# Kernel optimization log

Hardware: AMD Instinct MI355X
Metric: run time of the kernel (lower is better)

The kernel has to match this reference:

```python
import jax, jax.numpy as jnp
import numpy as np

E, N, D = 640000, 10000, 128  # edges, nodes, feature dim (edge=node=global=128)
H, O = 256, 128               # MLP hidden / output dims; concat dim = 4*D = 512


def setup_inputs() -> dict:
    key = jax.random.key(0)
    ks = jax.random.split(key, 7)
    return {
        "edge_attr": jax.random.normal(ks[0], (E, D), dtype=jnp.float32),
        "node_attr": jax.random.normal(ks[1], (N, D), dtype=jnp.float32),
        "global_attr": jax.random.normal(ks[2], (D,), dtype=jnp.float32),
        "senders": jax.random.randint(ks[3], (E,), 0, N),
        "receivers": jax.random.randint(ks[4], (E,), 0, N),
        "W1": jax.random.normal(ks[5], (4 * D, H), dtype=jnp.float32) / np.float32(np.sqrt(4 * D)),
        "b1": jnp.zeros((H,), dtype=jnp.float32),
        "W2": jax.random.normal(ks[6], (H, O), dtype=jnp.float32) / np.float32(np.sqrt(H)),
        "b2": jnp.zeros((O,), dtype=jnp.float32),
    }


def reference(edge_attr, node_attr, global_attr, senders, receivers, W1, b1, W2, b2):
    # Batched form of the per-edge Python loop:
    #   cat([e.data, e.receiver.data, e.sender.data, G.global_attribute.data]) -> updater MLP
    num_edges = edge_attr.shape[0]
    g = jnp.broadcast_to(global_attr, (num_edges, global_attr.shape[0]))  # [E, Dg]
    x = jnp.concatenate(
        [edge_attr, node_attr[receivers], node_attr[senders], g], axis=-1
    )  # [E, 4D]
    h = jax.nn.relu(x @ W1 + b1)  # [E, H]
    return h @ W2 + b2            # [E, O] : updated edge attributes
```

## Files before the change

kernel.cpp:

```cpp
#include <hip/hip_runtime.h>
#include <hip/hip_bf16.h>


typedef __attribute__((ext_vector_type(8))) short bf16x8;
typedef __attribute__((ext_vector_type(4))) float f32x4;

static __device__ __forceinline__ unsigned short f2bf(float f) {
    unsigned u = __builtin_bit_cast(unsigned, f);
    u += 0x7FFFu + ((u >> 16) & 1u);
    return (unsigned short)(u >> 16);
}


__global__ void prep_node_kernel(const float* __restrict__ node,
                                 ushort* __restrict__ nb) {
    int i = blockIdx.x * 256 + threadIdx.x;
    if (i >= 160000) return;
    const float4* s = (const float4*)(node + (size_t)i * 8);
    float4 a = s[0], b = s[1];
    ushort tmp[8] = { f2bf(a.x), f2bf(a.y), f2bf(a.z), f2bf(a.w),
                      f2bf(b.x), f2bf(b.y), f2bf(b.z), f2bf(b.w) };
    *(bf16x8*)&nb[(size_t)i * 8] = *(bf16x8*)tmp;
}

__global__ void prep_w1_kernel(const float* __restrict__ W1,
                               ushort* __restrict__ w1f) {
    int id = blockIdx.x * 256 + threadIdx.x;
    if (id >= 16 * 12 * 64) return;
    int l = id & 63, blk = id >> 6;
    int ks = blk % 12, gnt = blk / 12;
    int n  = gnt * 16 + (l & 15);
    int k0 = ks * 32 + (l >> 4) * 8;
    ushort tmp[8];
    #pragma unroll
    for (int j = 0; j < 8; ++j) tmp[j] = f2bf(W1[(k0 + j) * 256 + n]);
    *(bf16x8*)&w1f[(size_t)id * 8] = *(bf16x8*)tmp;
}

__global__ void prep_w2_kernel(const float* __restrict__ W2,
                               ushort* __restrict__ w2f) {
    int id = blockIdx.x * 256 + threadIdx.x;
    if (id >= 8 * 8 * 64) return;
    int l = id & 63, blk = id >> 6;
    int ks = blk % 8, gnt = blk / 8;
    int n  = gnt * 16 + (l & 15);
    int k0 = ks * 32 + (l >> 4) * 8;
    ushort tmp[8];
    #pragma unroll
    for (int j = 0; j < 8; ++j) tmp[j] = f2bf(W2[(k0 + j) * 128 + n]);
    *(bf16x8*)&w2f[(size_t)id * 8] = *(bf16x8*)tmp;
}

__global__ void prep_hbias_kernel(const float* __restrict__ W1,
                                  const float* __restrict__ b1,
                                  const float* __restrict__ g,
                                  float* __restrict__ hbias) {
    int n = threadIdx.x;
    float acc = b1[n];
    for (int k = 0; k < 128; ++k) acc += g[k] * W1[(384 + k) * 256 + n];
    hbias[n] = acc;
}


__global__ __launch_bounds__(256, 2) void edge_mlp_kernel(
    const float* __restrict__ edge_attr,
    const int* __restrict__ senders,
    const int* __restrict__ receivers,
    const ushort* __restrict__ node_bf,
    const ushort* __restrict__ w1f,
    const ushort* __restrict__ w2f,
    const float* __restrict__ hbias,
    const float* __restrict__ b2,
    float* __restrict__ out)
{
    __shared__ ushort Xe[64 * 128];
    __shared__ ushort Hs[64 * 256];

    const int t   = threadIdx.x;
    const int l   = t & 63;
    const int wid = t >> 6;
    const int base = blockIdx.x * 64;

    const int lr = l & 15;
    const int lk = (l >> 4) * 8;

    #pragma unroll
    for (int p = 0; p < 4; ++p) {
        int chunk = p * 256 + t;
        int r  = chunk >> 4;
        int c0 = (chunk & 15) * 8;
        const float4* src = (const float4*)(edge_attr + (size_t)(base + r) * 128 + c0);
        float4 a = src[0];
        float4 b = src[1];
        ushort tmp[8] = { f2bf(a.x), f2bf(a.y), f2bf(a.z), f2bf(a.w),
                          f2bf(b.x), f2bf(b.y), f2bf(b.z), f2bf(b.w) };
        *(bf16x8*)&Xe[r * 128 + (c0 ^ ((r & 7) << 3))] = *(bf16x8*)tmp;
    }

    int nrow[4], srow[4];
    #pragma unroll
    for (int mt = 0; mt < 4; ++mt) {
        int e = base + mt * 16 + lr;
        nrow[mt] = receivers[e] * 128;
        srow[mt] = senders[e]   * 128;
    }

    __syncthreads();

    f32x4 acc[4][4];
    #pragma unroll
    for (int mt = 0; mt < 4; ++mt)
        #pragma unroll
        for (int nt = 0; nt < 4; ++nt)
            acc[mt][nt] = (f32x4){0.f, 0.f, 0.f, 0.f};

    #pragma unroll
    for (int ks = 0; ks < 12; ++ks) {
        bf16x8 B[4];
        #pragma unroll
        for (int nt = 0; nt < 4; ++nt) {
            int gnt = wid * 4 + nt;
            B[nt] = *(const bf16x8*)&w1f[(size_t)((gnt * 12 + ks) * 64 + l) * 8];
        }
        bf16x8 A[4];
        const int seg = ks >> 2;
        const int kk  = (ks & 3) * 32 + lk;
        if (seg == 0) {
            #pragma unroll
            for (int mt = 0; mt < 4; ++mt) {
                int row = mt * 16 + lr;
                A[mt] = *(const bf16x8*)&Xe[row * 128 + (kk ^ ((row & 7) << 3))];
            }
        } else if (seg == 1) {
            #pragma unroll
            for (int mt = 0; mt < 4; ++mt)
                A[mt] = *(const bf16x8*)&node_bf[nrow[mt] + kk];
        } else {
            #pragma unroll
            for (int mt = 0; mt < 4; ++mt)
                A[mt] = *(const bf16x8*)&node_bf[srow[mt] + kk];
        }
        #pragma unroll
        for (int mt = 0; mt < 4; ++mt)
            #pragma unroll
            for (int nt = 0; nt < 4; ++nt)
                acc[mt][nt] = __builtin_amdgcn_mfma_f32_16x16x32_bf16(
                    A[mt], B[nt], acc[mt][nt], 0, 0, 0);
    }

    float hb[4];
    #pragma unroll
    for (int nt = 0; nt < 4; ++nt)
        hb[nt] = hbias[wid * 64 + nt * 16 + lr];

    #pragma unroll
    for (int mt = 0; mt < 4; ++mt)
        #pragma unroll
        for (int nt = 0; nt < 4; ++nt)
            #pragma unroll
            for (int j = 0; j < 4; ++j) {
                float v = acc[mt][nt][j] + hb[nt];
                v = fmaxf(v, 0.0f);
                int row = mt * 16 + (l >> 4) * 4 + j;
                int col = wid * 64 + nt * 16 + lr;
                Hs[row * 256 + (col ^ ((row & 7) << 3))] = f2bf(v);
            }

    __syncthreads();

    f32x4 acc2[4][2];
    #pragma unroll
    for (int mt = 0; mt < 4; ++mt)
        #pragma unroll
        for (int nt = 0; nt < 2; ++nt)
            acc2[mt][nt] = (f32x4){0.f, 0.f, 0.f, 0.f};

    #pragma unroll
    for (int ks = 0; ks < 8; ++ks) {
        bf16x8 B2[2];
        #pragma unroll
        for (int nt = 0; nt < 2; ++nt) {
            int gnt = wid * 2 + nt;
            B2[nt] = *(const bf16x8*)&w2f[(size_t)((gnt * 8 + ks) * 64 + l) * 8];
        }
        bf16x8 A2[4];
        const int kk = ks * 32 + lk;
        #pragma unroll
        for (int mt = 0; mt < 4; ++mt) {
            int row = mt * 16 + lr;
            A2[mt] = *(const bf16x8*)&Hs[row * 256 + (kk ^ ((row & 7) << 3))];
        }
        #pragma unroll
        for (int mt = 0; mt < 4; ++mt)
            #pragma unroll
            for (int nt = 0; nt < 2; ++nt)
                acc2[mt][nt] = __builtin_amdgcn_mfma_f32_16x16x32_bf16(
                    A2[mt], B2[nt], acc2[mt][nt], 0, 0, 0);
    }

    float b2v[2];
    #pragma unroll
    for (int nt = 0; nt < 2; ++nt)
        b2v[nt] = b2[wid * 32 + nt * 16 + lr];

    #pragma unroll
    for (int mt = 0; mt < 4; ++mt)
        #pragma unroll
        for (int nt = 0; nt < 2; ++nt)
            #pragma unroll
            for (int j = 0; j < 4; ++j) {
                int row = base + mt * 16 + (l >> 4) * 4 + j;
                int col = wid * 32 + nt * 16 + lr;
                out[(size_t)row * 128 + col] = acc2[mt][nt][j] + b2v[nt];
            }
}


extern "C" void kernel_launch(void* const* d_in, const int* in_sizes, int n_in,
                              void* d_out, int out_size, void* d_ws, size_t ws_size,
                              hipStream_t stream) {
    (void)in_sizes; (void)n_in; (void)out_size; (void)ws_size;

    const float* edge_attr   = (const float*)d_in[0];
    const float* node_attr   = (const float*)d_in[1];
    const float* global_attr = (const float*)d_in[2];
    const int*   senders     = (const int*)d_in[3];
    const int*   receivers   = (const int*)d_in[4];
    const float* W1          = (const float*)d_in[5];
    const float* b1          = (const float*)d_in[6];
    const float* W2          = (const float*)d_in[7];
    const float* b2          = (const float*)d_in[8];
    float* out = (float*)d_out;

    ushort* node_bf = (ushort*)d_ws;
    ushort* w1f     = (ushort*)((char*)d_ws + 2560000);
    ushort* w2f     = (ushort*)((char*)d_ws + 2756608);
    float*  hbias   = (float*)((char*)d_ws + 2822144);

    hipLaunchKernelGGL(prep_node_kernel,  dim3(625), dim3(256), 0, stream, node_attr, node_bf);
    hipLaunchKernelGGL(prep_w1_kernel,    dim3(48),  dim3(256), 0, stream, W1, w1f);
    hipLaunchKernelGGL(prep_w2_kernel,    dim3(16),  dim3(256), 0, stream, W2, w2f);
    hipLaunchKernelGGL(prep_hbias_kernel, dim3(1),   dim3(256), 0, stream, W1, b1, global_attr, hbias);

    hipLaunchKernelGGL(edge_mlp_kernel, dim3(10000), dim3(256), 0, stream,
                       edge_attr, senders, receivers, node_bf, w1f, w2f, hbias, b2, out);
}
```

Baseline: 350.0 us.

## Swap MFMA operands for vectorized epilogues and load edge features directly to registers

New measurement: 505.0 us. 44.3% more time.

```diff
diff --git a/kernel.cpp b/kernel.cpp
--- a/kernel.cpp
+++ b/kernel.cpp
@@ -4,11 +4,18 @@
 
 typedef __attribute__((ext_vector_type(8))) short bf16x8;
 typedef __attribute__((ext_vector_type(4))) float f32x4;
+typedef __attribute__((ext_vector_type(2))) unsigned int u32x2;
 
 static __device__ __forceinline__ unsigned short f2bf(float f) {
     unsigned u = __builtin_bit_cast(unsigned, f);
     u += 0x7FFFu + ((u >> 16) & 1u);
     return (unsigned short)(u >> 16);
+}
+
+static __device__ __forceinline__ unsigned cvt_pk_bf16(float lo, float hi) {
+    unsigned r;
+    asm("v_cvt_pk_bf16_f32 %0, %1, %2" : "=v"(r) : "v"(lo), "v"(hi));
+    return r;
 }
 
 
@@ -62,7 +69,7 @@
 }
 
 
-__global__ __launch_bounds__(256, 2) void edge_mlp_kernel(
+__global__ __launch_bounds__(256, 4) void edge_mlp_kernel(
     const float* __restrict__ edge_attr,
     const int* __restrict__ senders,
     const int* __restrict__ receivers,
@@ -73,29 +80,16 @@
     const float* __restrict__ b2,
     float* __restrict__ out)
 {
-    __shared__ ushort Xe[64 * 128];
     __shared__ ushort Hs[64 * 256];
 
-    const int t   = threadIdx.x;
-    const int l   = t & 63;
-    const int wid = t >> 6;
+    const int t    = threadIdx.x;
+    const int l    = t & 63;
+    const int wid  = t >> 6;
     const int base = blockIdx.x * 64;
 
     const int lr = l & 15;
-    const int lk = (l >> 4) * 8;
-
-    #pragma unroll
-    for (int p = 0; p < 4; ++p) {
-        int chunk = p * 256 + t;
-        int r  = chunk >> 4;
-        int c0 = (chunk & 15) * 8;
-        const float4* src = (const float4*)(edge_attr + (size_t)(base + r) * 128 + c0);
-        float4 a = src[0];
-        float4 b = src[1];
-        ushort tmp[8] = { f2bf(a.x), f2bf(a.y), f2bf(a.z), f2bf(a.w),
-                          f2bf(b.x), f2bf(b.y), f2bf(b.z), f2bf(b.w) };
-        *(bf16x8*)&Xe[r * 128 + (c0 ^ ((r & 7) << 3))] = *(bf16x8*)tmp;
-    }
+    const int q  = l >> 4;
+    const int lk = q * 8;
 
     int nrow[4], srow[4];
     #pragma unroll
@@ -105,8 +99,6 @@
         srow[mt] = senders[e]   * 128;
     }
 
-    __syncthreads();
-
     f32x4 acc[4][4];
     #pragma unroll
     for (int mt = 0; mt < 4; ++mt)
@@ -115,56 +107,63 @@
             acc[mt][nt] = (f32x4){0.f, 0.f, 0.f, 0.f};
 
     #pragma unroll
-    for (int ks = 0; ks < 12; ++ks) {
+    for (int ks = 0; ks < 4; ++ks) {
         bf16x8 B[4];
         #pragma unroll
-        for (int nt = 0; nt < 4; ++nt) {
-            int gnt = wid * 4 + nt;
-            B[nt] = *(const bf16x8*)&w1f[(size_t)((gnt * 12 + ks) * 64 + l) * 8];
-        }
-        bf16x8 A[4];
-        const int seg = ks >> 2;
-        const int kk  = (ks & 3) * 32 + lk;
-        if (seg == 0) {
-            #pragma unroll
-            for (int mt = 0; mt < 4; ++mt) {
-                int row = mt * 16 + lr;
-                A[mt] = *(const bf16x8*)&Xe[row * 128 + (kk ^ ((row & 7) << 3))];
-            }
-        } else if (seg == 1) {
-            #pragma unroll
-            for (int mt = 0; mt < 4; ++mt)
-                A[mt] = *(const bf16x8*)&node_bf[nrow[mt] + kk];
-        } else {
-            #pragma unroll
-            for (int mt = 0; mt < 4; ++mt)
-                A[mt] = *(const bf16x8*)&node_bf[srow[mt] + kk];
+        for (int nt = 0; nt < 4; ++nt)
+            B[nt] = *(const bf16x8*)&w1f[(size_t)(((wid * 4 + nt) * 12 + ks) * 64 + l) * 8];
+        bf16x8 X[4];
+        #pragma unroll
+        for (int mt = 0; mt < 4; ++mt) {
+            const float4* p = (const float4*)(edge_attr
+                + (size_t)(base + mt * 16 + lr) * 128 + ks * 32 + lk);
+            float4 a = p[0], b = p[1];
+            uint4 uu = { cvt_pk_bf16(a.x, a.y), cvt_pk_bf16(a.z, a.w),
+                         cvt_pk_bf16(b.x, b.y), cvt_pk_bf16(b.z, b.w) };
+            X[mt] = __builtin_bit_cast(bf16x8, uu);
         }
         #pragma unroll
         for (int mt = 0; mt < 4; ++mt)
             #pragma unroll
             for (int nt = 0; nt < 4; ++nt)
                 acc[mt][nt] = __builtin_amdgcn_mfma_f32_16x16x32_bf16(
-                    A[mt], B[nt], acc[mt][nt], 0, 0, 0);
-    }
-
-    float hb[4];
-    #pragma unroll
-    for (int nt = 0; nt < 4; ++nt)
-        hb[nt] = hbias[wid * 64 + nt * 16 + lr];
-
-    #pragma unroll
-    for (int mt = 0; mt < 4; ++mt)
+                    B[nt], X[mt], acc[mt][nt], 0, 0, 0);
+    }
+
+    #pragma unroll
+    for (int ks = 4; ks < 12; ++ks) {
+        bf16x8 B[4];
         #pragma unroll
         for (int nt = 0; nt < 4; ++nt)
+            B[nt] = *(const bf16x8*)&w1f[(size_t)(((wid * 4 + nt) * 12 + ks) * 64 + l) * 8];
+        const int off = ((ks - 4) & 3) * 32 + lk;
+        bf16x8 X[4];
+        #pragma unroll
+        for (int mt = 0; mt < 4; ++mt)
+            X[mt] = *(const bf16x8*)&node_bf[(ks < 8 ? nrow[mt] : srow[mt]) + off];
+        #pragma unroll
+        for (int mt = 0; mt < 4; ++mt)
             #pragma unroll
-            for (int j = 0; j < 4; ++j) {
-                float v = acc[mt][nt][j] + hb[nt];
-                v = fmaxf(v, 0.0f);
-                int row = mt * 16 + (l >> 4) * 4 + j;
-                int col = wid * 64 + nt * 16 + lr;
-                Hs[row * 256 + (col ^ ((row & 7) << 3))] = f2bf(v);
-            }
+            for (int nt = 0; nt < 4; ++nt)
+                acc[mt][nt] = __builtin_amdgcn_mfma_f32_16x16x32_bf16(
+                    B[nt], X[mt], acc[mt][nt], 0, 0, 0);
+    }
+
+    #pragma unroll
+    for (int nt = 0; nt < 4; ++nt) {
+        const int F = wid * 64 + nt * 16 + q * 4;
+        float4 hb4 = *(const float4*)&hbias[F];
+        #pragma unroll
+        for (int mt = 0; mt < 4; ++mt) {
+            float v0 = fmaxf(acc[mt][nt][0] + hb4.x, 0.f);
+            float v1 = fmaxf(acc[mt][nt][1] + hb4.y, 0.f);
+            float v2 = fmaxf(acc[mt][nt][2] + hb4.z, 0.f);
+            float v3 = fmaxf(acc[mt][nt][3] + hb4.w, 0.f);
+            u32x2 w = { cvt_pk_bf16(v0, v1), cvt_pk_bf16(v2, v3) };
+            const int edge = mt * 16 + lr;
+            *(u32x2*)&Hs[edge * 256 + (F ^ ((edge & 7) << 3))] = w;
+        }
+    }
 
     __syncthreads();
 
@@ -177,42 +176,36 @@
 
     #pragma unroll
     for (int ks = 0; ks < 8; ++ks) {
-        bf16x8 B2[2];
-        #pragma unroll
-        for (int nt = 0; nt < 2; ++nt) {
-            int gnt = wid * 2 + nt;
-            B2[nt] = *(const bf16x8*)&w2f[(size_t)((gnt * 8 + ks) * 64 + l) * 8];
-        }
-        bf16x8 A2[4];
-        const int kk = ks * 32 + lk;
-        #pragma unroll
-        for (int mt = 0; mt < 4; ++mt) {
-            int row = mt * 16 + lr;
-            A2[mt] = *(const bf16x8*)&Hs[row * 256 + (kk ^ ((row & 7) << 3))];
+        bf16x8 W[2];
+        #pragma unroll
+        for (int nt = 0; nt < 2; ++nt)
+            W[nt] = *(const bf16x8*)&w2f[(size_t)(((wid * 2 + nt) * 8 + ks) * 64 + l) * 8];
+        bf16x8 Hfr[4];
+        const int F = ks * 32 + lk;
+        #pragma unroll
+        for (int mt = 0; mt < 4; ++mt) {
+            const int edge = mt * 16 + lr;
+            Hfr[mt] = *(const bf16x8*)&Hs[edge * 256 + (F ^ ((edge & 7) << 3))];
         }
         #pragma unroll
         for (int mt = 0; mt < 4; ++mt)
             #pragma unroll
             for (int nt = 0; nt < 2; ++nt)
                 acc2[mt][nt] = __builtin_amdgcn_mfma_f32_16x16x32_bf16(
-                    A2[mt], B2[nt], acc2[mt][nt], 0, 0, 0);
-    }
-
-    float b2v[2];
-    #pragma unroll
-    for (int nt = 0; nt < 2; ++nt)
-        b2v[nt] = b2[wid * 32 + nt * 16 + lr];
-
-    #pragma unroll
-    for (int mt = 0; mt < 4; ++mt)
-        #pragma unroll
-        for (int nt = 0; nt < 2; ++nt)
-            #pragma unroll
-            for (int j = 0; j < 4; ++j) {
-                int row = base + mt * 16 + (l >> 4) * 4 + j;
-                int col = wid * 32 + nt * 16 + lr;
-                out[(size_t)row * 128 + col] = acc2[mt][nt][j] + b2v[nt];
-            }
+                    W[nt], Hfr[mt], acc2[mt][nt], 0, 0, 0);
+    }
+
+    #pragma unroll
+    for (int nt = 0; nt < 2; ++nt) {
+        const int F = wid * 32 + nt * 16 + q * 4;
+        float4 b24 = *(const float4*)&b2[F];
+        #pragma unroll
+        for (int mt = 0; mt < 4; ++mt) {
+            float4 o = { acc2[mt][nt][0] + b24.x, acc2[mt][nt][1] + b24.y,
+                         acc2[mt][nt][2] + b24.z, acc2[mt][nt][3] + b24.w };
+            *(float4*)&out[(size_t)(base + mt * 16 + lr) * 128 + F] = o;
+        }
+    }
 }
 
 
```
